# Optimization experiments

Hardware: AMD Instinct MI355X
Metric: run time of the kernel (lower is better)

Reference implementation:

```python
import jax, jax.numpy as jnp
import numpy as np

B, N, D = 4, 2048, 512
OUT, H = 512, 8
HD = OUT // H

def setup_inputs() -> dict:
    key = jax.random.key(0)
    ks = jax.random.split(key, 10)
    s = 1.0 / np.sqrt(D)
    x = jax.random.normal(ks[0], (B, N, D), dtype=jnp.float32)
    adj = jax.random.randint(ks[1], (N, N), 0, 2, dtype=jnp.int32)
    Wq = jax.random.uniform(ks[2], (D, OUT), jnp.float32, -s, s)
    bq = jax.random.uniform(ks[3], (OUT,), jnp.float32, -s, s)
    Wk = jax.random.uniform(ks[4], (D, OUT), jnp.float32, -s, s)
    bk = jax.random.uniform(ks[5], (OUT,), jnp.float32, -s, s)
    Wv = jax.random.uniform(ks[6], (D, OUT), jnp.float32, -s, s)
    bv = jax.random.uniform(ks[7], (OUT,), jnp.float32, -s, s)
    so = 1.0 / np.sqrt(OUT)
    Wo = jax.random.uniform(ks[8], (OUT, OUT), jnp.float32, -so, so)
    bo = jax.random.uniform(ks[9], (OUT,), jnp.float32, -so, so)
    return {"x": x, "adj": adj, "Wq": Wq, "bq": bq, "Wk": Wk, "bk": bk,
            "Wv": Wv, "bv": bv, "Wo": Wo, "bo": bo}

def reference(x, adj, Wq, bq, Wk, bk, Wv, bv, Wo, bo):
    scale = HD ** -0.5
    # [B,N,OUT] -> [B,H,N,HD]
    def split_heads(t):
        return t.reshape(B, N, H, HD).transpose(0, 2, 1, 3)
    q = split_heads(x @ Wq + bq)
    k = split_heads(x @ Wk + bk)
    v = split_heads(x @ Wv + bv)
    attn = jnp.einsum('bhnd,bhmd->bhnm', q, k) * scale  # [B,H,N,N]
    mask = (adj == 0)[None, None, :, :]
    attn = jnp.where(mask, jnp.float32(-1e9), attn)
    attn = jax.nn.softmax(attn, axis=-1)
    out = jnp.einsum('bhnm,bhmd->bhnd', attn, v)
    out = out.transpose(0, 2, 1, 3).reshape(B, N, OUT)
    return out @ Wo + bo
```

## Files before the change

### kernel.cpp

```cpp
#include <hip/hip_runtime.h>
#include <math.h>

#define NB   4
#define NN   2048
#define DD   512
#define NOUT 512
#define NH   8
#define HDIM 64

typedef __attribute__((ext_vector_type(4))) short bf16x4;
typedef __attribute__((ext_vector_type(8))) short bf16x8;
typedef __attribute__((ext_vector_type(4))) float f32x4;
#define MFMA32(a, b, c)  __builtin_amdgcn_mfma_f32_16x16x32_bf16(a, b, c, 0, 0, 0)

typedef const __attribute__((address_space(1))) unsigned int* gas_ptr;
typedef __attribute__((address_space(3))) unsigned int* las_ptr;

#define SCALE2 0.18033688f


__device__ inline unsigned short f2bf(float f) {
    unsigned int u = __float_as_uint(f);
    u += 0x7fffu + ((u >> 16) & 1u);
    return (unsigned short)(u >> 16);
}

__device__ inline unsigned int pack_trunc(float lo, float hi) {
    return __builtin_amdgcn_perm(__float_as_uint(hi), __float_as_uint(lo), 0x07060302u);
}

__global__ __launch_bounds__(256) void prep(
    const float* __restrict__ x, unsigned short* __restrict__ xt,
    const float* __restrict__ W0, const float* __restrict__ W1,
    const float* __restrict__ W2, const float* __restrict__ W3,
    unsigned short* __restrict__ Tqkv, unsigned short* __restrict__ To,
    const int* __restrict__ adj, unsigned int* __restrict__ amaskW)
{
    const int blk = blockIdx.x;
    const int t   = threadIdx.x;

    if (blk < 2048) {
        const int i = (blk * 256 + t) * 8;
        const int m = i >> 9, k = i & 511;
        float4 a = *(const float4*)(x + i);
        float4 b = *(const float4*)(x + i + 4);
        ushort4 u0, u1;
        u0.x = f2bf(a.x); u0.y = f2bf(a.y); u0.z = f2bf(a.z); u0.w = f2bf(a.w);
        u1.x = f2bf(b.x); u1.y = f2bf(b.y); u1.z = f2bf(b.z); u1.w = f2bf(b.w);
        unsigned short* dst = xt + ((size_t)(m >> 7) * 65536)
                                 + (k >> 5) * 4096 + (m & 127) * 32 + (k & 31);
        *(ushort4*)dst       = u0;
        *(ushort4*)(dst + 4) = u1;
        return;
    }
    if (blk < 2304) {
        __shared__ float tile[64][65];
        const int idx = blk - 2048;
        const int z = idx >> 6, rem = idx & 63;
        const float* W;
        switch (z) {
            case 0:  W = W0; break;
            case 1:  W = W1; break;
            case 2:  W = W2; break;
            default: W = W3; break;
        }
        unsigned short* T = (z < 3) ? Tqkv : To;
        const int ngbase  = (z < 3) ? z * 512 : 0;
        const int k0 = (rem & 7) * 64, n0 = (rem >> 3) * 64;
        const int r = t >> 6, c = t & 63;
#pragma unroll
        for (int rep = 0; rep < 16; ++rep) {
            const int row = rep * 4 + r;
            tile[row][c] = W[(size_t)(k0 + row) * NOUT + n0 + c];
        }
        __syncthreads();
        const int k  = k0 + c;
        const int ks = k >> 5, kk = k & 31;
#pragma unroll
        for (int rep = 0; rep < 16; ++rep) {
            const int row = rep * 4 + r;
            const int ng  = ngbase + n0 + row;
            T[((size_t)(ng >> 7) * 65536) + ks * 4096 + (ng & 127) * 32 + kk]
                = f2bf(tile[c][row]);
        }
        return;
    }
    {
        const int gid  = (blk - 2304) * 256 + t;
        const int w0   = gid * 4;
        const int qrow = w0 >> 10;
        const int wloc = w0 & 1023;
        const int kb0  = wloc * 2;
        int4 a0 = *(const int4*)(adj + (size_t)qrow * NN + kb0);
        int4 a1 = *(const int4*)(adj + (size_t)qrow * NN + kb0 + 4);
        uint4 m;
        m.x = (a0.x ? 0xFFFFu : 0u) | (a0.y ? 0xFFFF0000u : 0u);
        m.y = (a0.z ? 0xFFFFu : 0u) | (a0.w ? 0xFFFF0000u : 0u);
        m.z = (a1.x ? 0xFFFFu : 0u) | (a1.y ? 0xFFFF0000u : 0u);
        m.w = (a1.z ? 0xFFFFu : 0u) | (a1.w ? 0xFFFF0000u : 0u);
        *(uint4*)(amaskW + (size_t)qrow * 1024 + wloc) = m;
    }
}

#define GT_SETUP(Atil, Wtil)                                                   \
    const int t = threadIdx.x, wave = t >> 6, lane = t & 63;                   \
    const int quad = lane >> 4, l16 = lane & 15;                               \
    const int n0 = blockIdx.x * 128, m0 = blockIdx.y * 128;                    \
    const int wm = (wave & 1) * 64, wn = (wave >> 1) * 64;                     \
    const unsigned short* aP[4];                                               \
    const unsigned short* bP[4];                                               \
    _Pragma("unroll")                                                          \
    for (int mt = 0; mt < 4; ++mt)                                             \
        aP[mt] = Atil + (size_t)blockIdx.y * 65536                             \
               + (wm + mt * 16 + l16) * 32 + quad * 8;                         \
    _Pragma("unroll")                                                          \
    for (int nt = 0; nt < 4; ++nt)                                             \
        bP[nt] = Wtil + (size_t)blockIdx.x * 65536                             \
               + (wn + nt * 16 + l16) * 32 + quad * 8;

#define GT_LOADF(Af, Bf, NTC, ks)                                              \
    _Pragma("unroll")                                                          \
    for (int mt = 0; mt < 4; ++mt) Af[mt] = *(const bf16x8*)(aP[mt] + (ks) * 4096); \
    _Pragma("unroll")                                                          \
    for (int nt = 0; nt < NTC; ++nt) Bf[nt] = *(const bf16x8*)(bP[nt] + (ks) * 4096);

#define GT_MFMA(Af, Bf, NTC)                                                   \
    _Pragma("unroll")                                                          \
    for (int mt = 0; mt < 4; ++mt)                                             \
        _Pragma("unroll")                                                      \
        for (int nt = 0; nt < NTC; ++nt)                                       \
            acc[mt][nt] = MFMA32(Af[mt], Bf[nt], acc[mt][nt]);

#define GT_LOOP(NTC)                                                           \
    f32x4 acc[4][NTC];                                                         \
    _Pragma("unroll")                                                          \
    for (int mt = 0; mt < 4; ++mt)                                             \
        _Pragma("unroll")                                                      \
        for (int nt = 0; nt < NTC; ++nt) acc[mt][nt] = (f32x4){0.f, 0.f, 0.f, 0.f}; \
    bf16x8 aA[4], bA[NTC], aB[4], bB[NTC];                                     \
    GT_LOADF(aA, bA, NTC, 0);                                                  \
    for (int kk = 0; kk < 8; ++kk) {                                           \
        GT_LOADF(aB, bB, NTC, 2 * kk + 1);                                     \
        GT_MFMA(aA, bA, NTC);                                                  \
        if (kk < 7) { GT_LOADF(aA, bA, NTC, 2 * kk + 2); }                     \
        GT_MFMA(aB, bB, NTC);                                                  \
    }

__global__ __launch_bounds__(256, 3) void gemm_qkv(
    const unsigned short* __restrict__ Atil,
    const unsigned short* __restrict__ Wtil,
    const float* __restrict__ bq, const float* __restrict__ bk,
    const float* __restrict__ bv,
    unsigned short* __restrict__ qo, unsigned short* __restrict__ ko,
    unsigned short* __restrict__ vto)
{
    __shared__ unsigned short eps[4 * 2560];
    GT_SETUP(Atil, Wtil);
    GT_LOOP(4);

    const int seg   = n0 >> 9;
    const int nloc0 = n0 & 511;
    const float* bp = (seg == 0) ? bq : (seg == 1) ? bk : bv;
    unsigned short* dst3 = (seg == 0) ? qo : (seg == 1) ? ko : vto;
    const int h = (nloc0 + wn) >> 6;

    float bias4[4];
#pragma unroll
    for (int nt = 0; nt < 4; ++nt) bias4[nt] = bp[nloc0 + wn + nt * 16 + l16];

    unsigned short* Lo = eps + wave * 2560;
#pragma unroll
    for (int mt = 0; mt < 4; ++mt) {
        if (seg < 2) {
#pragma unroll
            for (int nt = 0; nt < 4; ++nt)
#pragma unroll
                for (int r = 0; r < 4; ++r) {
                    float val = acc[mt][nt][r] + bias4[nt];
                    if (seg == 0) val *= SCALE2;
                    Lo[(quad * 4 + r) * 72 + nt * 16 + l16] = f2bf(val);
                }
#pragma unroll
            for (int pass = 0; pass < 2; ++pass) {
                const int row = pass * 8 + (lane >> 3);
                const int mg  = m0 + wm + mt * 16 + row;
                const int bb  = mg >> 11, n = mg & (NN - 1);
                bf16x8 v = *(const bf16x8*)&Lo[row * 72 + (lane & 7) * 8];
                *(bf16x8*)(dst3 + ((size_t)(bb * NH + h) * NN + n) * HDIM
                           + (lane & 7) * 8) = v;
            }
        } else {
#pragma unroll
            for (int nt = 0; nt < 4; ++nt)
#pragma unroll
                for (int r = 0; r < 4; ++r) {
                    const float val = acc[mt][nt][r] + bias4[nt];
                    Lo[(nt * 16 + l16) * 40 + quad * 4 + r] = f2bf(val);
                }
            const int d  = lane;
            const int mg = m0 + wm + mt * 16;
            const int bb = mg >> 11, n = mg & (NN - 1);
            unsigned short* dr = dst3 + ((size_t)(bb * NH + h) * HDIM + d) * NN + n;
            *(bf16x8*)dr       = *(const bf16x8*)&Lo[d * 40];
            *(bf16x8*)(dr + 8) = *(const bf16x8*)&Lo[d * 40 + 8];
        }
    }
}

__global__ __launch_bounds__(256, 3) void gemm_o(
    const unsigned short* __restrict__ Atil,
    const unsigned short* __restrict__ Wtil,
    const float* __restrict__ bias,
    float* __restrict__ C)
{
    const int t = threadIdx.x, wave = t >> 6, lane = t & 63;
    const int quad = lane >> 4, l16 = lane & 15;
    const int n0 = blockIdx.x * 64, m0 = blockIdx.y * 128;
    const int wm = (wave & 1) * 64, wn = (wave >> 1) * 32;
    const unsigned short* aP[4];
    const unsigned short* bP[2];
#pragma unroll
    for (int mt = 0; mt < 4; ++mt)
        aP[mt] = Atil + (size_t)blockIdx.y * 65536
               + (wm + mt * 16 + l16) * 32 + quad * 8;
#pragma unroll
    for (int nt = 0; nt < 2; ++nt)
        bP[nt] = Wtil + (size_t)(n0 >> 7) * 65536
               + ((n0 & 64) + wn + nt * 16 + l16) * 32 + quad * 8;

    GT_LOOP(2);

    float bias2[2];
#pragma unroll
    for (int nt = 0; nt < 2; ++nt) bias2[nt] = bias[n0 + wn + nt * 16 + l16];

#pragma unroll
    for (int mt = 0; mt < 4; ++mt)
#pragma unroll
        for (int nt = 0; nt < 2; ++nt) {
            const int col = n0 + wn + nt * 16 + l16;
#pragma unroll
            for (int r = 0; r < 4; ++r) {
                const int row = m0 + wm + mt * 16 + quad * 4 + r;
                C[(size_t)row * NOUT + col] = acc[mt][nt][r] + bias2[nt];
            }
        }
}

__global__ __launch_bounds__(512) void attn_mfma(
    const unsigned short* __restrict__ qg,
    const unsigned short* __restrict__ kg,
    const unsigned short* __restrict__ vt,
    const unsigned int* __restrict__ amask,
    unsigned short* __restrict__ aot)
{
    __shared__ unsigned short smem[4 * 64 * 64];
    unsigned short* Ka = smem;
    unsigned short* Va = smem + 4096;
    unsigned short* Kb = smem + 8192;
    unsigned short* Vb = smem + 12288;

    const int t    = threadIdx.x;
    const int wave = t >> 6;
    const int lane = t & 63;
    const int quad = lane >> 4;
    const int l16  = lane & 15;

    const int qt = blockIdx.x, h = blockIdx.y, b = blockIdx.z;
    const int bh = b * NH + h;
    const int q0 = qt * 128;

    const unsigned short* kbase  = kg + (size_t)bh * NN * HDIM;
    const unsigned short* vtbase = vt + (size_t)bh * HDIM * NN;

    const int drow = lane >> 3;
    const int dblk = (lane & 7) ^ drow;
    const int p  = wave * 8 + drow;
    const int Lp = (p & 32) + ((p >> 2) & 3) * 8 + ((p >> 4) & 1) * 4 + (p & 3);

    const int sw  = l16 & 7;
    const int bo0 = (quad ^ sw) * 8;
    const int bo1 = bo0 ^ 32;

#define ATT_ISSUE(kt, Kd, Vd)                                                  \
    {                                                                          \
        const int r0 = wave * 8;                                               \
        __builtin_amdgcn_global_load_lds(                                      \
            (gas_ptr)(kbase + (size_t)((kt) * 64 + Lp) * HDIM + dblk * 8),     \
            (las_ptr)(Kd + r0 * 64), 16, 0, 0);                                \
        __builtin_amdgcn_global_load_lds(                                      \
            (gas_ptr)(vtbase + (size_t)(r0 + drow) * NN + (kt) * 64 + dblk * 8), \
            (las_ptr)(Vd + r0 * 64), 16, 0, 0);                                \
    }

    const int myq = q0 + wave * 16 + l16;
    const unsigned short* qrow = qg + ((size_t)bh * NN + myq) * HDIM;
    const bf16x8 bQ0 = *(const bf16x8*)(qrow + quad * 8);
    const bf16x8 bQ1 = *(const bf16x8*)(qrow + quad * 8 + 32);

    const unsigned int* mrow = amask + (size_t)myq * 1024 + quad * 4;
#define MLOAD(kt, c) (*(const uint4*)(mrow + (kt) * 32 + (c) * 16))

    bf16x8 ones8;
#pragma unroll
    for (int j = 0; j < 8; ++j) ones8[j] = (short)0x3F80;

    f32x4 O[4];
#pragma unroll
    for (int dt = 0; dt < 4; ++dt) O[dt] = (f32x4){0.f, 0.f, 0.f, 0.f};
    f32x4 lacc = (f32x4){0.f, 0.f, 0.f, 0.f};

    auto tile = [&](const unsigned short* Ks, const unsigned short* Vs,
                    uint4 mw0, uint4 mw1) {
        bf16x8 Pt[2];
#pragma unroll
        for (int c = 0; c < 2; ++c) {
            const uint4 mw = c ? mw1 : mw0;
            union { unsigned int u[4]; bf16x8 v; } cv;
#pragma unroll
            for (int half = 0; half < 2; ++half) {
                const int nt = c * 2 + half;
                bf16x8 aK0 = *(const bf16x8*)&Ks[(nt * 16 + l16) * 64 + bo0];
                bf16x8 aK1 = *(const bf16x8*)&Ks[(nt * 16 + l16) * 64 + bo1];
                f32x4 s = (f32x4){0.f, 0.f, 0.f, 0.f};
                s = MFMA32(aK0, bQ0, s);
                s = MFMA32(aK1, bQ1, s);
                const float p0 = exp2f(s[0]);
                const float p1 = exp2f(s[1]);
                const float p2 = exp2f(s[2]);
                const float p3 = exp2f(s[3]);
                cv.u[half * 2 + 0] = pack_trunc(p0, p1) & (half ? mw.z : mw.x);
                cv.u[half * 2 + 1] = pack_trunc(p2, p3) & (half ? mw.w : mw.y);
            }
            Pt[c] = cv.v;
            lacc = MFMA32(ones8, Pt[c], lacc);
        }
#pragma unroll
        for (int dt = 0; dt < 4; ++dt)
#pragma unroll
            for (int c = 0; c < 2; ++c) {
                bf16x8 aV = *(const bf16x8*)
                    &Vs[(dt * 16 + l16) * 64 + (((c * 4 + quad) ^ sw) * 8)];
                O[dt] = MFMA32(aV, Pt[c], O[dt]);
            }
    };

    uint4 mA0 = MLOAD(0, 0), mA1 = MLOAD(0, 1);
    uint4 mB0, mB1;
    ATT_ISSUE(0, Ka, Va);
    for (int kk = 0; kk < 16; ++kk) {
        __syncthreads();
        ATT_ISSUE(2 * kk + 1, Kb, Vb);
        mB0 = MLOAD(2 * kk + 1, 0); mB1 = MLOAD(2 * kk + 1, 1);
        tile(Ka, Va, mA0, mA1);
        __syncthreads();
        if (kk < 15) {
            ATT_ISSUE(2 * kk + 2, Ka, Va);
            mA0 = MLOAD(2 * kk + 2, 0); mA1 = MLOAD(2 * kk + 2, 1);
        }
        tile(Kb, Vb, mB0, mB1);
    }
    __syncthreads();

    const float inv = 1.f / lacc[0];
    unsigned short* Lo = smem + wave * (16 * 72);
#pragma unroll
    for (int dt = 0; dt < 4; ++dt) {
        const float v0 = O[dt][0] * inv, v1 = O[dt][1] * inv;
        const float v2 = O[dt][2] * inv, v3 = O[dt][3] * inv;
        *(unsigned int*)&Lo[l16 * 72 + dt * 16 + quad * 4]     = pack_trunc(v0, v1);
        *(unsigned int*)&Lo[l16 * 72 + dt * 16 + quad * 4 + 2] = pack_trunc(v2, v3);
    }
    const int rr = lane >> 2;
    const int qq = q0 + wave * 16 + rr;
    const int m  = b * NN + qq;
    const int mb = m >> 7, r = m & 127;
#pragma unroll
    for (int i = 0; i < 2; ++i) {
        const int ch = (lane & 3) + 4 * i;
        const int ks = h * 2 + (ch >> 2);
        bf16x8 val = *(const bf16x8*)&Lo[rr * 72 + ch * 8];
        *(bf16x8*)(aot + (size_t)mb * 65536 + ks * 4096 + r * 32 + (ch & 3) * 8) = val;
    }
#undef ATT_ISSUE
#undef MLOAD
}

extern "C" void kernel_launch(void* const* d_in, const int* in_sizes, int n_in,
                              void* d_out, int out_size, void* d_ws, size_t ws_size,
                              hipStream_t stream)
{
    const float* x   = (const float*)d_in[0];
    const int*   adj = (const int*)  d_in[1];
    const float* Wq  = (const float*)d_in[2];
    const float* bq  = (const float*)d_in[3];
    const float* Wk  = (const float*)d_in[4];
    const float* bk  = (const float*)d_in[5];
    const float* Wv  = (const float*)d_in[6];
    const float* bv  = (const float*)d_in[7];
    const float* Wo  = (const float*)d_in[8];
    const float* bo  = (const float*)d_in[9];
    float* out = (float*)d_out;

    const size_t qkv_elems = (size_t)NB * NH * NN * HDIM;
    unsigned short* xt    = (unsigned short*)d_ws;
    unsigned short* q     = xt   + qkv_elems;
    unsigned short* kb    = q    + qkv_elems;
    unsigned short* vtb   = kb   + qkv_elems;
    unsigned short* tWqkv = vtb  + qkv_elems;
    unsigned short* tWo   = tWqkv + (size_t)3 * DD * NOUT;
    unsigned int*   amaskW = (unsigned int*)(tWo + (size_t)DD * NOUT);
    unsigned short* aot   = xt;

    prep<<<dim3(4352), 256, 0, stream>>>(x, xt, Wq, Wk, Wv, Wo,
                                         tWqkv, tWo, adj, amaskW);

    gemm_qkv<<<dim3(12, 64), 256, 0, stream>>>(xt, tWqkv, bq, bk, bv, q, kb, vtb);

    attn_mfma<<<dim3(NN / 128, NH, NB), 512, 0, stream>>>(q, kb, vtb, amaskW, aot);

    gemm_o<<<dim3(8, 64), 256, 0, stream>>>(aot, tWo, bo, out);
}
```

Before: 195.9 us.

## Give each attention wave two query tiles and narrow QKV GEMM tiles

The attention kernel now runs with 256 threads, and each wave handles 32 query rows as two 16-row groups. Every K and V fragment read from LDS is reused across both groups, which halves LDS fragment traffic per MFMA but doubles the per-wave register state for the accumulators and masks. The QKV GEMM changes to 128x64 block tiles with twice the grid, which raises parallelism. The shared GEMM loop now uses a triple-buffered register prefetch with full unrolling, and gemm_o reuses the same setup macro.

```diff
diff --git a/kernel.cpp b/kernel.cpp
--- a/kernel.cpp
+++ b/kernel.cpp
@@ -102,48 +102,49 @@
     }
 }
 
-#define GT_SETUP(Atil, Wtil)                                                   \
+#define GT_SETUP64()                                                           \
     const int t = threadIdx.x, wave = t >> 6, lane = t & 63;                   \
     const int quad = lane >> 4, l16 = lane & 15;                               \
-    const int n0 = blockIdx.x * 128, m0 = blockIdx.y * 128;                    \
-    const int wm = (wave & 1) * 64, wn = (wave >> 1) * 64;                     \
+    const int n0 = blockIdx.x * 64, m0 = blockIdx.y * 128;                     \
+    const int wm = (wave & 1) * 64, wn = (wave >> 1) * 32;                     \
     const unsigned short* aP[4];                                               \
-    const unsigned short* bP[4];                                               \
+    const unsigned short* bP[2];                                               \
     _Pragma("unroll")                                                          \
     for (int mt = 0; mt < 4; ++mt)                                             \
         aP[mt] = Atil + (size_t)blockIdx.y * 65536                             \
                + (wm + mt * 16 + l16) * 32 + quad * 8;                         \
     _Pragma("unroll")                                                          \
-    for (int nt = 0; nt < 4; ++nt)                                             \
-        bP[nt] = Wtil + (size_t)blockIdx.x * 65536                             \
-               + (wn + nt * 16 + l16) * 32 + quad * 8;
-
-#define GT_LOADF(Af, Bf, NTC, ks)                                              \
+    for (int nt = 0; nt < 2; ++nt) {                                           \
+        const int ng = n0 + wn + nt * 16 + l16;                                \
+        bP[nt] = Wtil + (size_t)(ng >> 7) * 65536 + (ng & 127) * 32 + quad * 8; \
+    }
+
+#define GT_LOADF(Af, Bf, ks)                                                   \
     _Pragma("unroll")                                                          \
     for (int mt = 0; mt < 4; ++mt) Af[mt] = *(const bf16x8*)(aP[mt] + (ks) * 4096); \
     _Pragma("unroll")                                                          \
-    for (int nt = 0; nt < NTC; ++nt) Bf[nt] = *(const bf16x8*)(bP[nt] + (ks) * 4096);
-
-#define GT_MFMA(Af, Bf, NTC)                                                   \
+    for (int nt = 0; nt < 2; ++nt) Bf[nt] = *(const bf16x8*)(bP[nt] + (ks) * 4096);
+
+#define GT_MFMA(Af, Bf)                                                        \
     _Pragma("unroll")                                                          \
     for (int mt = 0; mt < 4; ++mt)                                             \
         _Pragma("unroll")                                                      \
-        for (int nt = 0; nt < NTC; ++nt)                                       \
+        for (int nt = 0; nt < 2; ++nt)                                         \
             acc[mt][nt] = MFMA32(Af[mt], Bf[nt], acc[mt][nt]);
 
-#define GT_LOOP(NTC)                                                           \
-    f32x4 acc[4][NTC];                                                         \
+#define GT_LOOP3()                                                             \
+    f32x4 acc[4][2];                                                           \
     _Pragma("unroll")                                                          \
     for (int mt = 0; mt < 4; ++mt)                                             \
         _Pragma("unroll")                                                      \
-        for (int nt = 0; nt < NTC; ++nt) acc[mt][nt] = (f32x4){0.f, 0.f, 0.f, 0.f}; \
-    bf16x8 aA[4], bA[NTC], aB[4], bB[NTC];                                     \
-    GT_LOADF(aA, bA, NTC, 0);                                                  \
-    for (int kk = 0; kk < 8; ++kk) {                                           \
-        GT_LOADF(aB, bB, NTC, 2 * kk + 1);                                     \
-        GT_MFMA(aA, bA, NTC);                                                  \
-        if (kk < 7) { GT_LOADF(aA, bA, NTC, 2 * kk + 2); }                     \
-        GT_MFMA(aB, bB, NTC);                                                  \
+        for (int nt = 0; nt < 2; ++nt) acc[mt][nt] = (f32x4){0.f, 0.f, 0.f, 0.f}; \
+    bf16x8 aS[3][4], bS[3][2];                                                 \
+    GT_LOADF(aS[0], bS[0], 0);                                                 \
+    GT_LOADF(aS[1], bS[1], 1);                                                 \
+    _Pragma("unroll")                                                          \
+    for (int kk = 0; kk < 16; ++kk) {                                          \
+        if (kk < 14) { GT_LOADF(aS[(kk + 2) % 3], bS[(kk + 2) % 3], kk + 2); } \
+        GT_MFMA(aS[kk % 3], bS[kk % 3]);                                       \
     }
 
 __global__ __launch_bounds__(256, 3) void gemm_qkv(
@@ -154,9 +155,9 @@
     unsigned short* __restrict__ qo, unsigned short* __restrict__ ko,
     unsigned short* __restrict__ vto)
 {
-    __shared__ unsigned short eps[4 * 2560];
-    GT_SETUP(Atil, Wtil);
-    GT_LOOP(4);
+    __shared__ unsigned short eps[4 * 768];
+    GT_SETUP64();
+    GT_LOOP3();
 
     const int seg   = n0 >> 9;
     const int nloc0 = n0 & 511;
@@ -164,45 +165,42 @@
     unsigned short* dst3 = (seg == 0) ? qo : (seg == 1) ? ko : vto;
     const int h = (nloc0 + wn) >> 6;
 
-    float bias4[4];
-#pragma unroll
-    for (int nt = 0; nt < 4; ++nt) bias4[nt] = bp[nloc0 + wn + nt * 16 + l16];
-
-    unsigned short* Lo = eps + wave * 2560;
+    float bias2[2];
+#pragma unroll
+    for (int nt = 0; nt < 2; ++nt) bias2[nt] = bp[nloc0 + wn + nt * 16 + l16];
+
+    unsigned short* Lo = eps + wave * 768;
 #pragma unroll
     for (int mt = 0; mt < 4; ++mt) {
         if (seg < 2) {
 #pragma unroll
-            for (int nt = 0; nt < 4; ++nt)
+            for (int nt = 0; nt < 2; ++nt)
 #pragma unroll
                 for (int r = 0; r < 4; ++r) {
-                    float val = acc[mt][nt][r] + bias4[nt];
+                    float val = acc[mt][nt][r] + bias2[nt];
                     if (seg == 0) val *= SCALE2;
-                    Lo[(quad * 4 + r) * 72 + nt * 16 + l16] = f2bf(val);
+                    Lo[(quad * 4 + r) * 40 + nt * 16 + l16] = f2bf(val);
                 }
-#pragma unroll
-            for (int pass = 0; pass < 2; ++pass) {
-                const int row = pass * 8 + (lane >> 3);
-                const int mg  = m0 + wm + mt * 16 + row;
-                const int bb  = mg >> 11, n = mg & (NN - 1);
-                bf16x8 v = *(const bf16x8*)&Lo[row * 72 + (lane & 7) * 8];
-                *(bf16x8*)(dst3 + ((size_t)(bb * NH + h) * NN + n) * HDIM
-                           + (lane & 7) * 8) = v;
-            }
+            const int row = lane >> 2;
+            const int mg  = m0 + wm + mt * 16 + row;
+            const int bb  = mg >> 11, n = mg & (NN - 1);
+            bf16x8 v = *(const bf16x8*)&Lo[row * 40 + (lane & 3) * 8];
+            *(bf16x8*)(dst3 + ((size_t)(bb * NH + h) * NN + n) * HDIM
+                       + wn + (lane & 3) * 8) = v;
         } else {
 #pragma unroll
-            for (int nt = 0; nt < 4; ++nt)
+            for (int nt = 0; nt < 2; ++nt)
 #pragma unroll
                 for (int r = 0; r < 4; ++r) {
-                    const float val = acc[mt][nt][r] + bias4[nt];
-                    Lo[(nt * 16 + l16) * 40 + quad * 4 + r] = f2bf(val);
+                    const float val = acc[mt][nt][r] + bias2[nt];
+                    Lo[(nt * 16 + l16) * 24 + quad * 4 + r] = f2bf(val);
                 }
-            const int d  = lane;
+            const int d  = lane >> 1;
             const int mg = m0 + wm + mt * 16;
             const int bb = mg >> 11, n = mg & (NN - 1);
-            unsigned short* dr = dst3 + ((size_t)(bb * NH + h) * HDIM + d) * NN + n;
-            *(bf16x8*)dr       = *(const bf16x8*)&Lo[d * 40];
-            *(bf16x8*)(dr + 8) = *(const bf16x8*)&Lo[d * 40 + 8];
+            bf16x8 v = *(const bf16x8*)&Lo[d * 24 + (lane & 1) * 8];
+            *(bf16x8*)(dst3 + ((size_t)(bb * NH + h) * HDIM + wn + d) * NN
+                       + n + (lane & 1) * 8) = v;
         }
     }
 }
@@ -213,22 +211,8 @@
     const float* __restrict__ bias,
     float* __restrict__ C)
 {
-    const int t = threadIdx.x, wave = t >> 6, lane = t & 63;
-    const int quad = lane >> 4, l16 = lane & 15;
-    const int n0 = blockIdx.x * 64, m0 = blockIdx.y * 128;
-    const int wm = (wave & 1) * 64, wn = (wave >> 1) * 32;
-    const unsigned short* aP[4];
-    const unsigned short* bP[2];
-#pragma unroll
-    for (int mt = 0; mt < 4; ++mt)
-        aP[mt] = Atil + (size_t)blockIdx.y * 65536
-               + (wm + mt * 16 + l16) * 32 + quad * 8;
-#pragma unroll
-    for (int nt = 0; nt < 2; ++nt)
-        bP[nt] = Wtil + (size_t)(n0 >> 7) * 65536
-               + ((n0 & 64) + wn + nt * 16 + l16) * 32 + quad * 8;
-
-    GT_LOOP(2);
+    GT_SETUP64();
+    GT_LOOP3();
 
     float bias2[2];
 #pragma unroll
@@ -247,7 +231,7 @@
         }
 }
 
-__global__ __launch_bounds__(512) void attn_mfma(
+__global__ __launch_bounds__(256, 2) void attn_mfma(
     const unsigned short* __restrict__ qg,
     const unsigned short* __restrict__ kg,
     const unsigned short* __restrict__ vt,
@@ -275,65 +259,85 @@
 
     const int drow = lane >> 3;
     const int dblk = (lane & 7) ^ drow;
-    const int p  = wave * 8 + drow;
-    const int Lp = (p & 32) + ((p >> 2) & 3) * 8 + ((p >> 4) & 1) * 4 + (p & 3);
 
     const int sw  = l16 & 7;
     const int bo0 = (quad ^ sw) * 8;
     const int bo1 = bo0 ^ 32;
 
 #define ATT_ISSUE(kt, Kd, Vd)                                                  \
-    {                                                                          \
-        const int r0 = wave * 8;                                               \
+    _Pragma("unroll")                                                          \
+    for (int c = 0; c < 2; ++c) {                                              \
+        const int r0 = wave * 16 + c * 8;                                      \
+        const int p  = r0 + drow;                                              \
+        const int Lp = (p & 32) + ((p >> 2) & 3) * 8 + ((p >> 4) & 1) * 4 + (p & 3); \
         __builtin_amdgcn_global_load_lds(                                      \
             (gas_ptr)(kbase + (size_t)((kt) * 64 + Lp) * HDIM + dblk * 8),     \
             (las_ptr)(Kd + r0 * 64), 16, 0, 0);                                \
         __builtin_amdgcn_global_load_lds(                                      \
-            (gas_ptr)(vtbase + (size_t)(r0 + drow) * NN + (kt) * 64 + dblk * 8), \
+            (gas_ptr)(vtbase + (size_t)p * NN + (kt) * 64 + dblk * 8),         \
             (las_ptr)(Vd + r0 * 64), 16, 0, 0);                                \
     }
 
-    const int myq = q0 + wave * 16 + l16;
-    const unsigned short* qrow = qg + ((size_t)bh * NN + myq) * HDIM;
-    const bf16x8 bQ0 = *(const bf16x8*)(qrow + quad * 8);
-    const bf16x8 bQ1 = *(const bf16x8*)(qrow + quad * 8 + 32);
-
-    const unsigned int* mrow = amask + (size_t)myq * 1024 + quad * 4;
-#define MLOAD(kt, c) (*(const uint4*)(mrow + (kt) * 32 + (c) * 16))
+    const int myq0 = q0 + wave * 32 + l16;
+    const int myq1 = myq0 + 16;
+    const unsigned short* qr0 = qg + ((size_t)bh * NN + myq0) * HDIM;
+    const unsigned short* qr1 = qg + ((size_t)bh * NN + myq1) * HDIM;
+    bf16x8 bQ0[2], bQ1[2];
+    bQ0[0] = *(const bf16x8*)(qr0 + quad * 8);
+    bQ1[0] = *(const bf16x8*)(qr0 + quad * 8 + 32);
+    bQ0[1] = *(const bf16x8*)(qr1 + quad * 8);
+    bQ1[1] = *(const bf16x8*)(qr1 + quad * 8 + 32);
+
+    const unsigned int* mrow[2] = {
+        amask + (size_t)myq0 * 1024 + quad * 4,
+        amask + (size_t)myq1 * 1024 + quad * 4 };
+
+#define MLOADG(dst, kt)                                                        \
+    _Pragma("unroll")                                                          \
+    for (int g = 0; g < 2; ++g)                                                \
+        _Pragma("unroll")                                                      \
+        for (int c = 0; c < 2; ++c)                                            \
+            dst[g * 2 + c] = *(const uint4*)(mrow[g] + (kt) * 32 + c * 16);
 
     bf16x8 ones8;
 #pragma unroll
     for (int j = 0; j < 8; ++j) ones8[j] = (short)0x3F80;
 
-    f32x4 O[4];
-#pragma unroll
-    for (int dt = 0; dt < 4; ++dt) O[dt] = (f32x4){0.f, 0.f, 0.f, 0.f};
-    f32x4 lacc = (f32x4){0.f, 0.f, 0.f, 0.f};
+    f32x4 O[2][4];
+#pragma unroll
+    for (int g = 0; g < 2; ++g)
+#pragma unroll
+        for (int dt = 0; dt < 4; ++dt) O[g][dt] = (f32x4){0.f, 0.f, 0.f, 0.f};
+    f32x4 lacc[2];
+    lacc[0] = (f32x4){0.f, 0.f, 0.f, 0.f};
+    lacc[1] = (f32x4){0.f, 0.f, 0.f, 0.f};
 
     auto tile = [&](const unsigned short* Ks, const unsigned short* Vs,
-                    uint4 mw0, uint4 mw1) {
-        bf16x8 Pt[2];
-#pragma unroll
-        for (int c = 0; c < 2; ++c) {
-            const uint4 mw = c ? mw1 : mw0;
-            union { unsigned int u[4]; bf16x8 v; } cv;
-#pragma unroll
-            for (int half = 0; half < 2; ++half) {
-                const int nt = c * 2 + half;
-                bf16x8 aK0 = *(const bf16x8*)&Ks[(nt * 16 + l16) * 64 + bo0];
-                bf16x8 aK1 = *(const bf16x8*)&Ks[(nt * 16 + l16) * 64 + bo1];
+                    const uint4* mw) {
+        union { unsigned int u[2][4]; bf16x8 v[2]; } P[2];
+#pragma unroll
+        for (int nt = 0; nt < 4; ++nt) {
+            bf16x8 aK0 = *(const bf16x8*)&Ks[(nt * 16 + l16) * 64 + bo0];
+            bf16x8 aK1 = *(const bf16x8*)&Ks[(nt * 16 + l16) * 64 + bo1];
+            const int c = nt >> 1, half = nt & 1;
+#pragma unroll
+            for (int g = 0; g < 2; ++g) {
                 f32x4 s = (f32x4){0.f, 0.f, 0.f, 0.f};
-                s = MFMA32(aK0, bQ0, s);
-                s = MFMA32(aK1, bQ1, s);
+                s = MFMA32(aK0, bQ0[g], s);
+                s = MFMA32(aK1, bQ1[g], s);
                 const float p0 = exp2f(s[0]);
                 const float p1 = exp2f(s[1]);
                 const float p2 = exp2f(s[2]);
                 const float p3 = exp2f(s[3]);
-                cv.u[half * 2 + 0] = pack_trunc(p0, p1) & (half ? mw.z : mw.x);
-                cv.u[half * 2 + 1] = pack_trunc(p2, p3) & (half ? mw.w : mw.y);
+                const uint4 m = mw[g * 2 + c];
+                P[g].u[c][half * 2 + 0] = pack_trunc(p0, p1) & (half ? m.z : m.x);
+                P[g].u[c][half * 2 + 1] = pack_trunc(p2, p3) & (half ? m.w : m.y);
             }
-            Pt[c] = cv.v;
-            lacc = MFMA32(ones8, Pt[c], lacc);
+        }
+#pragma unroll
+        for (int g = 0; g < 2; ++g) {
+            lacc[g] = MFMA32(ones8, P[g].v[0], lacc[g]);
+            lacc[g] = MFMA32(ones8, P[g].v[1], lacc[g]);
         }
 #pragma unroll
         for (int dt = 0; dt < 4; ++dt)
@@ -341,49 +345,54 @@
             for (int c = 0; c < 2; ++c) {
                 bf16x8 aV = *(const bf16x8*)
                     &Vs[(dt * 16 + l16) * 64 + (((c * 4 + quad) ^ sw) * 8)];
-                O[dt] = MFMA32(aV, Pt[c], O[dt]);
+#pragma unroll
+                for (int g = 0; g < 2; ++g)
+                    O[g][dt] = MFMA32(aV, P[g].v[c], O[g][dt]);
             }
     };
 
-    uint4 mA0 = MLOAD(0, 0), mA1 = MLOAD(0, 1);
-    uint4 mB0, mB1;
+    uint4 mA[4], mB[4];
+    MLOADG(mA, 0);
     ATT_ISSUE(0, Ka, Va);
     for (int kk = 0; kk < 16; ++kk) {
         __syncthreads();
         ATT_ISSUE(2 * kk + 1, Kb, Vb);
-        mB0 = MLOAD(2 * kk + 1, 0); mB1 = MLOAD(2 * kk + 1, 1);
-        tile(Ka, Va, mA0, mA1);
+        MLOADG(mB, 2 * kk + 1);
+        tile(Ka, Va, mA);
         __syncthreads();
         if (kk < 15) {
             ATT_ISSUE(2 * kk + 2, Ka, Va);
-            mA0 = MLOAD(2 * kk + 2, 0); mA1 = MLOAD(2 * kk + 2, 1);
-        }
-        tile(Kb, Vb, mB0, mB1);
+            MLOADG(mA, 2 * kk + 2);
+        }
+        tile(Kb, Vb, mB);
     }
     __syncthreads();
 
-    const float inv = 1.f / lacc[0];
     unsigned short* Lo = smem + wave * (16 * 72);
 #pragma unroll
-    for (int dt = 0; dt < 4; ++dt) {
-        const float v0 = O[dt][0] * inv, v1 = O[dt][1] * inv;
-        const float v2 = O[dt][2] * inv, v3 = O[dt][3] * inv;
-        *(unsigned int*)&Lo[l16 * 72 + dt * 16 + quad * 4]     = pack_trunc(v0, v1);
-        *(unsigned int*)&Lo[l16 * 72 + dt * 16 + quad * 4 + 2] = pack_trunc(v2, v3);
-    }
-    const int rr = lane >> 2;
-    const int qq = q0 + wave * 16 + rr;
-    const int m  = b * NN + qq;
-    const int mb = m >> 7, r = m & 127;
-#pragma unroll
-    for (int i = 0; i < 2; ++i) {
-        const int ch = (lane & 3) + 4 * i;
-        const int ks = h * 2 + (ch >> 2);
-        bf16x8 val = *(const bf16x8*)&Lo[rr * 72 + ch * 8];
-        *(bf16x8*)(aot + (size_t)mb * 65536 + ks * 4096 + r * 32 + (ch & 3) * 8) = val;
+    for (int g = 0; g < 2; ++g) {
+        const float inv = 1.f / lacc[g][0];
+#pragma unroll
+        for (int dt = 0; dt < 4; ++dt) {
+            const float v0 = O[g][dt][0] * inv, v1 = O[g][dt][1] * inv;
+            const float v2 = O[g][dt][2] * inv, v3 = O[g][dt][3] * inv;
+            *(unsigned int*)&Lo[l16 * 72 + dt * 16 + quad * 4]     = pack_trunc(v0, v1);
+            *(unsigned int*)&Lo[l16 * 72 + dt * 16 + quad * 4 + 2] = pack_trunc(v2, v3);
+        }
+        const int rr = lane >> 2;
+        const int qq = q0 + wave * 32 + g * 16 + rr;
+        const int m  = b * NN + qq;
+        const int mb = m >> 7, r = m & 127;
+#pragma unroll
+        for (int i = 0; i < 2; ++i) {
+            const int ch = (lane & 3) + 4 * i;
+            const int ks = h * 2 + (ch >> 2);
+            bf16x8 val = *(const bf16x8*)&Lo[rr * 72 + ch * 8];
+            *(bf16x8*)(aot + (size_t)mb * 65536 + ks * 4096 + r * 32 + (ch & 3) * 8) = val;
+        }
     }
 #undef ATT_ISSUE
-#undef MLOAD
+#undef MLOADG
 }
 
 extern "C" void kernel_launch(void* const* d_in, const int* in_sizes, int n_in,
@@ -415,9 +424,9 @@
     prep<<<dim3(4352), 256, 0, stream>>>(x, xt, Wq, Wk, Wv, Wo,
                                          tWqkv, tWo, adj, amaskW);
 
-    gemm_qkv<<<dim3(12, 64), 256, 0, stream>>>(xt, tWqkv, bq, bk, bv, q, kb, vtb);
-
-    attn_mfma<<<dim3(NN / 128, NH, NB), 512, 0, stream>>>(q, kb, vtb, amaskW, aot);
+    gemm_qkv<<<dim3(24, 64), 256, 0, stream>>>(xt, tWqkv, bq, bk, bv, q, kb, vtb);
+
+    attn_mfma<<<dim3(NN / 128, NH, NB), 256, 0, stream>>>(q, kb, vtb, amaskW, aot);
 
     gemm_o<<<dim3(8, 64), 256, 0, stream>>>(aot, tWo, bo, out);
 }
```

Measured after the change: 212.5 us. +8.5%, slower.
